# Kernel tuning notes

Hardware: AMD Instinct MI355X
Metric: run time of the kernel (lower is better)

Reference implementation:

```python
import jax, jax.numpy as jnp
import numpy as np

B, N, NF, K, C, L, IN_DIM, FC_DIM, OUT_DIM = 4, 4096, 8192, 512, 128, 4, 3, 128, 1


def setup_inputs() -> dict:
    rng = np.random.default_rng(0)
    key = jax.random.key(0)
    ks = jax.random.split(key, 10)
    # active-point indices inside the padded grid (unique, sorted) and matching mask
    ind = np.sort(rng.choice(NF, size=N, replace=False)).astype(np.int32)
    grid = rng.uniform(0.0, 2.0 * np.pi, size=(B, NF, 2)).astype(np.float32)
    w_quad = np.full((B, NF, 1), 1.0 / N, dtype=np.float32)
    mask = np.zeros((B, NF, 1), dtype=np.float32)
    mask[:, ind, 0] = 1.0
    xf = jnp.asarray(np.concatenate([grid, w_quad, mask], axis=-1))  # (B, NF, 4)
    x = jax.random.normal(ks[0], (B, N, IN_DIM), jnp.float32)
    modes = jnp.asarray(rng.integers(-16, 17, size=(K, 2)).astype(np.float32))
    scale = 1.0 / (C * C)
    wc = scale * jax.random.uniform(ks[1], (L, C, C, K), jnp.float32)
    ws_ = scale * jax.random.uniform(ks[2], (L, C, C, K), jnp.float32)
    w0 = scale * jax.random.uniform(ks[3], (L, C, C, 1), jnp.float32)
    conv_w = 0.05 * jax.random.normal(ks[4], (L, C, C), jnp.float32)
    conv_b = jnp.zeros((L, C), jnp.float32)
    fc0_w = 0.05 * jax.random.normal(ks[5], (IN_DIM, C), jnp.float32)
    fc0_b = jnp.zeros((C,), jnp.float32)
    fc1_w = 0.05 * jax.random.normal(ks[6], (C, FC_DIM), jnp.float32)
    fc1_b = jnp.zeros((FC_DIM,), jnp.float32)
    fc2_w = 0.05 * jax.random.normal(ks[7], (FC_DIM, OUT_DIM), jnp.float32)
    fc2_b = jnp.zeros((OUT_DIM,), jnp.float32)
    return dict(x=x, xf=xf, ind=jnp.asarray(ind), modes=modes,
                fc0_w=fc0_w, fc0_b=fc0_b, wc=wc, ws_=ws_, w0=w0,
                conv_w=conv_w, conv_b=conv_b, fc1_w=fc1_w, fc1_b=fc1_b,
                fc2_w=fc2_w, fc2_b=fc2_b)


def _gelu(v):
    # torch F.gelu default is the exact (erf) gelu
    return jax.nn.gelu(v, approximate=False)


def reference(x, xf, ind, modes, fc0_w, fc0_b, wc, ws_, w0, conv_w, conv_b,
              fc1_w, fc1_b, fc2_w, fc2_b):
    ndim = modes.shape[1]
    aux = jnp.transpose(xf[..., -2 - ndim:], (0, 2, 1))      # (B, ndim+2, NF)
    grid = aux[:, :ndim]                                       # (B, ndim, NF)
    wq = aux[:, ndim:ndim + 1]                                 # (B, 1, NF) quadrature weights
    temp = jnp.einsum('bdx,kd->bkx', grid, modes)              # (B, K, NF)
    bases_c, bases_s = jnp.cos(temp), jnp.sin(temp)
    bases_0 = jnp.ones((xf.shape[0], 1, xf.shape[1]), xf.dtype)
    size = ind.shape[0]                                        # count_nonzero(mask) == len(ind)
    wb_c = bases_c * (wq * size)
    wb_s = bases_s * (wq * size)
    wb_0 = bases_0 * (wq * size)
    # lift and scatter active points into the padded grid (done ONCE, as in the original)
    h = jnp.einsum('bni,ic->bcn', x[..., :fc0_w.shape[0]], fc0_w) + fc0_b[None, :, None]
    xg = jnp.zeros((x.shape[0], h.shape[1], xf.shape[1]), h.dtype).at[:, :, ind].set(h)
    nf = xg.shape[-1]
    n_layers = wc.shape[0]
    for i in range(n_layers):
        # forward non-uniform Fourier transform
        xch = jnp.einsum('bix,bkx->bik', xg, wb_c)
        xsh = -jnp.einsum('bix,bkx->bik', xg, wb_s)
        x0h = jnp.einsum('bix,bkx->bik', xg, wb_0)
        wci, wsi, w0i = wc[i] / nf, ws_[i] / nf, w0[i] / nf
        # complex-style mode mixing
        fch = jnp.einsum('bik,iok->bok', xch, wci) - jnp.einsum('bik,iok->bok', xsh, wsi)
        fsh = jnp.einsum('bik,iok->bok', xsh, wci) + jnp.einsum('bik,iok->bok', xch, wsi)
        f0h = jnp.einsum('bik,iok->bok', x0h, w0i)
        # inverse transform, then gather active points
        x1 = (jnp.einsum('bok,bkx->box', f0h, bases_0)
              + 2.0 * jnp.einsum('bok,bkx->box', fch, bases_c)
              - 2.0 * jnp.einsum('bok,bkx->box', fsh, bases_s))[:, :, ind]
        # 1x1 conv skip path on active points
        x2 = jnp.einsum('oi,bin->bon', conv_w[i], h) + conv_b[i][None, :, None]
        h = x1 + x2
        if i != n_layers - 1:
            h = _gelu(h)
    out = jnp.transpose(h, (0, 2, 1))                          # (B, N, C)
    out = _gelu(out @ fc1_w + fc1_b)
    out = out @ fc2_w + fc2_b                                  # (B, N, 1)
    return out
```

## Files before the change

### kernel.cpp

```cpp
#include <hip/hip_runtime.h>
#include <cmath>

#define B_ 4
#define N_ 4096
#define NF_ 8192
#define K_ 512
#define C_ 128
#define L_ 4
#define FCD_ 128
#define SPLIT_ 8

typedef _Float16 f16x8 __attribute__((ext_vector_type(8)));
typedef _Float16 f16x4 __attribute__((ext_vector_type(4)));
typedef float f32x4 __attribute__((ext_vector_type(4)));

#define MFMA16(a, b, c) __builtin_amdgcn_mfma_f32_16x16x32_f16((a), (b), (c), 0, 0, 0)

static const float SPLIT_SCALE = 2048.0f;
static const float INV_SPLIT_SCALE = 1.0f / 2048.0f;

static const size_t SZ_H   = (size_t)B_ * C_ * N_;
static const size_t SZ_HS  = (size_t)B_ * C_ * N_ / 2;
static const size_t SZ_FS  = (size_t)B_ * C_ * K_ / 2;
static const size_t SZ_CW  = (size_t)L_ * C_ * C_ / 2;
static const size_t SZ_W1  = (size_t)C_ * FCD_ / 2;

static const size_t H_OFF    = 0;
static const size_t H2_OFF   = H_OFF + SZ_H;
static const size_t HAH_OFF  = H2_OFF + SZ_H;
static const size_t HAL_OFF  = HAH_OFF + SZ_HS;
static const size_t HTH_OFF  = HAL_OFF + SZ_HS;
static const size_t HTL_OFF  = HTH_OFF + SZ_HS;
static const size_t WQN_OFF  = HTL_OFF + SZ_HS;
static const size_t GXY_OFF  = WQN_OFF + (size_t)B_ * N_;
static const size_t XCH_OFF  = GXY_OFF + (size_t)B_ * N_ * 2;
static const size_t XSH_OFF  = XCH_OFF + (size_t)B_ * C_ * K_;
static const size_t FCHH_OFF = XSH_OFF + (size_t)B_ * C_ * K_;
static const size_t FCHL_OFF = FCHH_OFF + SZ_FS;
static const size_t FSHH_OFF = FCHL_OFF + SZ_FS;
static const size_t FSHL_OFF = FSHH_OFF + SZ_FS;
static const size_t CWH_OFF  = FSHL_OFF + SZ_FS;
static const size_t CWL_OFF  = CWH_OFF + SZ_CW;
static const size_t X0_OFF   = CWL_OFF + SZ_CW;
static const size_t F0_OFF   = X0_OFF + (size_t)B_ * C_;
static const size_t XCP_OFF  = F0_OFF + (size_t)B_ * C_;
static const size_t XSP_OFF  = XCP_OFF + (size_t)SPLIT_ * B_ * C_ * K_;
static const size_t W1TH_OFF = XSP_OFF + (size_t)SPLIT_ * B_ * C_ * K_;
static const size_t W1TL_OFF = W1TH_OFF + SZ_W1;

__device__ __forceinline__ float gelu_exact(float v) {
    return v * 0.5f * (1.0f + erff(v * 0.70710678118654752440f));
}

__device__ __forceinline__ void fsplit(float v, _Float16& hi, _Float16& lo) {
    hi = (_Float16)v;
    lo = (_Float16)((v - (float)hi) * SPLIT_SCALE);
}

__global__ void prep_kernel(const float* __restrict__ x, const float* __restrict__ xf,
                            const int* __restrict__ ind, const float* __restrict__ fc0_w,
                            const float* __restrict__ fc0_b, float* __restrict__ h,
                            float* __restrict__ wqn, float* __restrict__ gxy) {
    int n = blockIdx.x * 256 + threadIdx.x;
    int c = blockIdx.y;
    int b = blockIdx.z;
    const float* xp = x + ((size_t)b * N_ + n) * 3;
    float acc = fc0_b[c] + xp[0] * fc0_w[0 * C_ + c] + xp[1] * fc0_w[1 * C_ + c]
              + xp[2] * fc0_w[2 * C_ + c];
    h[((size_t)b * C_ + c) * N_ + n] = acc;
    if (c == 0) {
        int g = ind[n];
        const float* xfp = xf + ((size_t)b * NF_ + g) * 4;
        wqn[b * N_ + n] = xfp[2] * (float)N_;
        gxy[((size_t)b * N_ + n) * 2 + 0] = xfp[0];
        gxy[((size_t)b * N_ + n) * 2 + 1] = xfp[1];
    }
}

__global__ void conv_split(const float* __restrict__ conv_w, _Float16* __restrict__ cwh,
                           _Float16* __restrict__ cwl) {
    int t = blockIdx.x * 256 + threadIdx.x;
    _Float16 hi, lo;
    fsplit(conv_w[t], hi, lo);
    cwh[t] = hi; cwl[t] = lo;
}

__global__ void w1_split(const float* __restrict__ fc1_w, _Float16* __restrict__ w1th,
                         _Float16* __restrict__ w1tl) {
    int t = blockIdx.x * 256 + threadIdx.x;
    int j = t >> 7, c = t & (C_ - 1);
    _Float16 hi, lo;
    fsplit(fc1_w[c * FCD_ + j], hi, lo);
    w1th[t] = hi; w1tl[t] = lo;
}

__device__ __forceinline__ unsigned int pack2(_Float16 a, _Float16 b) {
    union { _Float16 f[2]; unsigned int u; } x;
    x.f[0] = a; x.f[1] = b;
    return x.u;
}

__device__ __forceinline__ void unpack2(unsigned int v, _Float16& a, _Float16& b) {
    union { _Float16 f[2]; unsigned int u; } x;
    x.u = v;
    a = x.f[0]; b = x.f[1];
}

__global__ __launch_bounds__(256) void split_h(const float* __restrict__ h,
        const float* __restrict__ wqn, _Float16* __restrict__ hah,
        _Float16* __restrict__ hal, _Float16* __restrict__ hth,
        _Float16* __restrict__ htl) {
    __shared__ unsigned int pk[64][65];
    int tid = threadIdx.x;
    int n0 = blockIdx.x * 64, c0 = blockIdx.y * 64, b = blockIdx.z;
    int col = tid & 63, row4 = tid >> 6;
    for (int r = row4; r < 64; r += 4) {
        int c = c0 + r, n = n0 + col;
        float v = h[((size_t)b * C_ + c) * N_ + n];
        _Float16 ph, pl;
        fsplit(v, ph, pl);
        pk[r][col] = pack2(ph, pl);
        float a = v * wqn[b * N_ + n];
        _Float16 ah, al;
        fsplit(a, ah, al);
        size_t o = ((size_t)b * C_ + c) * N_ + n;
        hah[o] = ah; hal[o] = al;
    }
    __syncthreads();
    for (int r = row4; r < 64; r += 4) {
        int n = n0 + r, c = c0 + col;
        _Float16 ph, pl;
        unpack2(pk[col][r], ph, pl);
        size_t o = ((size_t)b * N_ + n) * C_ + c;
        hth[o] = ph; htl[o] = pl;
    }
}

__global__ __launch_bounds__(256) void fwd_mfma(const _Float16* __restrict__ hah,
        const _Float16* __restrict__ hal, const float* __restrict__ gxy,
        const float* __restrict__ modes, float* __restrict__ xcp,
        float* __restrict__ xsp) {
    __shared__ __align__(16) _Float16 tCH[2][32][40];
    __shared__ __align__(16) _Float16 tCL[2][32][40];
    __shared__ __align__(16) _Float16 tSH[2][32][40];
    __shared__ __align__(16) _Float16 tSL[2][32][40];
    __shared__ float gx_s[N_ / SPLIT_], gy_s[N_ / SPLIT_];
    int tid = threadIdx.x;
    int w = tid >> 6, lane = tid & 63, l15 = lane & 15, q = lane >> 4;
    int k0g = blockIdx.x * 32, p = blockIdx.y, b = blockIdx.z;
    int cstrip = w * 32;
    {
        const float* g = gxy + ((size_t)b * N_ + p * (N_ / SPLIT_)) * 2;
        float4 v = *(const float4*)(g + tid * 4);
        gx_s[tid * 2 + 0] = v.x; gy_s[tid * 2 + 0] = v.y;
        gx_s[tid * 2 + 1] = v.z; gy_s[tid * 2 + 1] = v.w;
    }
    int kk = tid & 31, ng = tid >> 5;
    float mx = modes[(k0g + kk) * 2 + 0];
    float my = modes[(k0g + kk) * 2 + 1];

    size_t arow[2];
    arow[0] = ((size_t)b * C_ + cstrip + l15) * N_;
    arow[1] = arow[0] + (size_t)16 * N_;
    f32x4 z = {0.f, 0.f, 0.f, 0.f};
    f32x4 aC1[2][2], aC2[2][2], aS1[2][2], aS2[2][2];
    for (int i = 0; i < 2; ++i)
        for (int j = 0; j < 2; ++j) {
            aC1[i][j] = z; aC2[i][j] = z; aS1[i][j] = z; aS2[i][j] = z;
        }

#define FWD_TILE(ITER, BUF) do {                                             \
        int nb_ = (ITER) * 32;                                               \
        f16x4 vch_, vcl_, vsh_, vsl_;                                        \
        for (int j_ = 0; j_ < 4; ++j_) {                                     \
            int nn_ = ng * 4 + j_;                                           \
            float t_ = gx_s[nb_ + nn_] * mx + gy_s[nb_ + nn_] * my;          \
            float s_, c_;                                                    \
            sincosf(t_, &s_, &c_);                                           \
            _Float16 h_, lo_;                                                \
            fsplit(c_, h_, lo_); vch_[j_] = h_; vcl_[j_] = lo_;              \
            fsplit(s_, h_, lo_); vsh_[j_] = h_; vsl_[j_] = lo_;              \
        }                                                                    \
        *(f16x4*)&tCH[BUF][kk][ng * 4] = vch_;                               \
        *(f16x4*)&tCL[BUF][kk][ng * 4] = vcl_;                               \
        *(f16x4*)&tSH[BUF][kk][ng * 4] = vsh_;                               \
        *(f16x4*)&tSL[BUF][kk][ng * 4] = vsl_;                               \
    } while (0)

    __syncthreads();
    FWD_TILE(0, 0);
    const int NIT = (N_ / SPLIT_) / 32;
    for (int it = 0; it < NIT; ++it) {
        __syncthreads();
        int cur = it & 1;
        int off = p * (N_ / SPLIT_) + it * 32 + q * 8;
        f16x8 ah[2], al[2];
        for (int mt = 0; mt < 2; ++mt) {
            ah[mt] = *(const f16x8*)(hah + arow[mt] + off);
            al[mt] = *(const f16x8*)(hal + arow[mt] + off);
        }
        f16x8 bch[2], bcl[2], bsh[2], bsl[2];
        for (int kt = 0; kt < 2; ++kt) {
            int r = kt * 16 + l15;
            bch[kt] = *(const f16x8*)&tCH[cur][r][q * 8];
            bcl[kt] = *(const f16x8*)&tCL[cur][r][q * 8];
            bsh[kt] = *(const f16x8*)&tSH[cur][r][q * 8];
            bsl[kt] = *(const f16x8*)&tSL[cur][r][q * 8];
        }
        if (it + 1 < NIT) FWD_TILE(it + 1, cur ^ 1);
        for (int mt = 0; mt < 2; ++mt)
            for (int kt = 0; kt < 2; ++kt) {
                aC1[mt][kt] = MFMA16(ah[mt], bch[kt], aC1[mt][kt]);
                aC2[mt][kt] = MFMA16(ah[mt], bcl[kt], aC2[mt][kt]);
                aC2[mt][kt] = MFMA16(al[mt], bch[kt], aC2[mt][kt]);
                aS1[mt][kt] = MFMA16(ah[mt], bsh[kt], aS1[mt][kt]);
                aS2[mt][kt] = MFMA16(ah[mt], bsl[kt], aS2[mt][kt]);
                aS2[mt][kt] = MFMA16(al[mt], bsh[kt], aS2[mt][kt]);
            }
    }
#undef FWD_TILE
    size_t pb = (size_t)p * B_ + b;
    for (int mt = 0; mt < 2; ++mt)
        for (int kt = 0; kt < 2; ++kt)
            for (int r = 0; r < 4; ++r) {
                int c = cstrip + mt * 16 + q * 4 + r;
                int k = k0g + kt * 16 + l15;
                size_t o = (pb * C_ + c) * K_ + k;
                xcp[o] = aC1[mt][kt][r] + aC2[mt][kt][r] * INV_SPLIT_SCALE;
                xsp[o] = -(aS1[mt][kt][r] + aS2[mt][kt][r] * INV_SPLIT_SCALE);
            }
}

__global__ void red_kernel(const float* __restrict__ xcp, const float* __restrict__ xsp,
                           float* __restrict__ xch, float* __restrict__ xsh) {
    int t = blockIdx.x * 256 + threadIdx.x;
    const int BCK = B_ * C_ * K_;
    float a = 0.f, s = 0.f;
    for (int p = 0; p < SPLIT_; ++p) {
        a += xcp[(size_t)p * BCK + t];
        s += xsp[(size_t)p * BCK + t];
    }
    xch[t] = a; xsh[t] = s;
}

__global__ void x0_kernel(const float* __restrict__ h, const float* __restrict__ wqn,
                          float* __restrict__ x0h) {
    int c = blockIdx.x, b = blockIdx.y;
    int tid = threadIdx.x;
    const float* hp = h + ((size_t)b * C_ + c) * N_;
    const float* wq = wqn + b * N_;
    float a = 0.f;
    for (int n = tid; n < N_; n += 256) a += hp[n] * wq[n];
    __shared__ float red[4];
    for (int off = 32; off; off >>= 1) a += __shfl_down(a, off, 64);
    if ((tid & 63) == 0) red[tid >> 6] = a;
    __syncthreads();
    if (tid == 0) x0h[b * C_ + c] = red[0] + red[1] + red[2] + red[3];
}

__global__ void f0_kernel(const float* __restrict__ x0h, const float* __restrict__ w0,
                          int l, float* __restrict__ f0h) {
    int o = threadIdx.x, b = blockIdx.x;
    const float* w = w0 + (size_t)l * C_ * C_;
    float a = 0.f;
    for (int i = 0; i < C_; ++i) a += x0h[b * C_ + i] * w[i * C_ + o];
    f0h[b * C_ + o] = a * (1.0f / NF_);
}

__global__ __launch_bounds__(256) void mix_kernel(const float* __restrict__ xch,
        const float* __restrict__ xsh, const float* __restrict__ wc,
        const float* __restrict__ ws, int l, _Float16* __restrict__ fchh,
        _Float16* __restrict__ fchl, _Float16* __restrict__ fshh,
        _Float16* __restrict__ fshl) {
    __shared__ float red[512 * 5];
    int tid = threadIdx.x;
    int lane = tid & 63;
    int g = tid >> 6;
    int k = blockIdx.x * 64 + lane;
    int o = blockIdx.y;
    const float* wcb = wc + ((size_t)l * C_ * C_ + o) * K_ + k;
    const float* wsb = ws + ((size_t)l * C_ * C_ + o) * K_ + k;
    float fc[4] = {0, 0, 0, 0}, fs[4] = {0, 0, 0, 0};
    int i0 = g * 32;
#pragma unroll 4
    for (int ii = 0; ii < 32; ++ii) {
        int i = i0 + ii;
        float wci = wcb[(size_t)i * (C_ * K_)];
        float wsi = wsb[(size_t)i * (C_ * K_)];
#pragma unroll
        for (int b = 0; b < 4; ++b) {
            float xc = xch[((size_t)b * C_ + i) * K_ + k];
            float xs = xsh[((size_t)b * C_ + i) * K_ + k];
            fc[b] += xc * wci - xs * wsi;
            fs[b] += xs * wci + xc * wsi;
        }
    }
#pragma unroll
    for (int b = 0; b < 4; ++b) {
        red[((b * 2 + 0) * 64 + lane) * 5 + g] = fc[b];
        red[((b * 2 + 1) * 64 + lane) * 5 + g] = fs[b];
    }
    __syncthreads();
    const float sc = 2.0f / NF_;
    for (int v = tid; v < 512; v += 256) {
        float sum = (red[v * 5 + 0] + red[v * 5 + 1] + red[v * 5 + 2] + red[v * 5 + 3]) * sc;
        int lane2 = v & 63;
        int bs = v >> 6;
        int b = bs >> 1, s = bs & 1;
        size_t idx = ((size_t)b * C_ + o) * K_ + blockIdx.x * 64 + lane2;
        _Float16 hi, lo;
        if (s == 0) {
            fsplit(sum, hi, lo);
            fchh[idx] = hi; fchl[idx] = lo;
        } else {
            fsplit(-sum, hi, lo);
            fshh[idx] = hi; fshl[idx] = lo;
        }
    }
}

__global__ __launch_bounds__(256) void inv_mfma(const _Float16* __restrict__ fchh,
        const _Float16* __restrict__ fchl, const _Float16* __restrict__ fshh,
        const _Float16* __restrict__ fshl, const float* __restrict__ gxy,
        const float* __restrict__ modes, const _Float16* __restrict__ cwh,
        const _Float16* __restrict__ cwl, const _Float16* __restrict__ hth,
        const _Float16* __restrict__ htl, const float* __restrict__ f0h,
        const float* __restrict__ conv_b, int l, int last, float* __restrict__ hnext) {
    __shared__ __align__(16) _Float16 tCH[2][32][40];
    __shared__ __align__(16) _Float16 tCL[2][32][40];
    __shared__ __align__(16) _Float16 tSH[2][32][40];
    __shared__ __align__(16) _Float16 tSL[2][32][40];
    __shared__ float mx_s[K_], my_s[K_];
    int tid = threadIdx.x;
    int w = tid >> 6, lane = tid & 63, l15 = lane & 15, q = lane >> 4;
    int n0g = blockIdx.x * 32, b = blockIdx.y;
    int cstrip = w * 32;
    {
        float4 v = *(const float4*)(modes + tid * 4);
        mx_s[tid * 2 + 0] = v.x; my_s[tid * 2 + 0] = v.y;
        mx_s[tid * 2 + 1] = v.z; my_s[tid * 2 + 1] = v.w;
    }
    int nn = tid & 31, kg = tid >> 5;
    float gx = gxy[((size_t)b * N_ + n0g + nn) * 2 + 0];
    float gy = gxy[((size_t)b * N_ + n0g + nn) * 2 + 1];

    size_t frow[2], nrow2[2], crow[2];
    frow[0] = ((size_t)b * C_ + cstrip + l15) * K_;
    frow[1] = frow[0] + (size_t)16 * K_;
    nrow2[0] = ((size_t)b * N_ + n0g + l15) * C_;
    nrow2[1] = nrow2[0] + (size_t)16 * C_;
    crow[0] = ((size_t)l * C_ + cstrip + l15) * C_;
    crow[1] = crow[0] + (size_t)16 * C_;
    f32x4 z = {0.f, 0.f, 0.f, 0.f};
    f32x4 a1[2][2], a2[2][2];
    for (int i = 0; i < 2; ++i)
        for (int j = 0; j < 2; ++j) { a1[i][j] = z; a2[i][j] = z; }

#define INV_TILE(KC, BUF) do {                                               \
        f16x4 vch_, vcl_, vsh_, vsl_;                                        \
        for (int j_ = 0; j_ < 4; ++j_) {                                     \
            int kk_ = (KC) + kg * 4 + j_;                                    \
            float t_ = gx * mx_s[kk_] + gy * my_s[kk_];                      \
            float s_, c_;                                                    \
            sincosf(t_, &s_, &c_);                                           \
            _Float16 h_, lo_;                                                \
            fsplit(c_, h_, lo_); vch_[j_] = h_; vcl_[j_] = lo_;              \
            fsplit(s_, h_, lo_); vsh_[j_] = h_; vsl_[j_] = lo_;              \
        }                                                                    \
        *(f16x4*)&tCH[BUF][nn][kg * 4] = vch_;                               \
        *(f16x4*)&tCL[BUF][nn][kg * 4] = vcl_;                               \
        *(f16x4*)&tSH[BUF][nn][kg * 4] = vsh_;                               \
        *(f16x4*)&tSL[BUF][nn][kg * 4] = vsl_;                               \
    } while (0)

    __syncthreads();
    INV_TILE(0, 0);
    const int NIT = K_ / 32;
    for (int it = 0; it < NIT; ++it) {
        __syncthreads();
        int cur = it & 1;
        int off = it * 32 + q * 8;
        f16x8 fch_[2], fcl_[2], fsh_[2], fsl_[2];
        for (int mt = 0; mt < 2; ++mt) {
            fch_[mt] = *(const f16x8*)(fchh + frow[mt] + off);
            fcl_[mt] = *(const f16x8*)(fchl + frow[mt] + off);
            fsh_[mt] = *(const f16x8*)(fshh + frow[mt] + off);
            fsl_[mt] = *(const f16x8*)(fshl + frow[mt] + off);
        }
        f16x8 bch[2], bcl[2], bsh[2], bsl[2];
        for (int nt = 0; nt < 2; ++nt) {
            int r = nt * 16 + l15;
            bch[nt] = *(const f16x8*)&tCH[cur][r][q * 8];
            bcl[nt] = *(const f16x8*)&tCL[cur][r][q * 8];
            bsh[nt] = *(const f16x8*)&tSH[cur][r][q * 8];
            bsl[nt] = *(const f16x8*)&tSL[cur][r][q * 8];
        }
        if (it + 1 < NIT) INV_TILE((it + 1) * 32, cur ^ 1);
        for (int mt = 0; mt < 2; ++mt)
            for (int nt = 0; nt < 2; ++nt) {
                a1[mt][nt] = MFMA16(fch_[mt], bch[nt], a1[mt][nt]);
                a2[mt][nt] = MFMA16(fch_[mt], bcl[nt], a2[mt][nt]);
                a2[mt][nt] = MFMA16(fcl_[mt], bch[nt], a2[mt][nt]);
                a1[mt][nt] = MFMA16(fsh_[mt], bsh[nt], a1[mt][nt]);
                a2[mt][nt] = MFMA16(fsh_[mt], bsl[nt], a2[mt][nt]);
                a2[mt][nt] = MFMA16(fsl_[mt], bsh[nt], a2[mt][nt]);
            }
    }
#undef INV_TILE
    for (int ic = 0; ic < C_; ic += 32) {
        int off = ic + q * 8;
        f16x8 awh[2], awl[2];
        for (int mt = 0; mt < 2; ++mt) {
            awh[mt] = *(const f16x8*)(cwh + crow[mt] + off);
            awl[mt] = *(const f16x8*)(cwl + crow[mt] + off);
        }
        f16x8 bhh[2], bhl[2];
        for (int nt = 0; nt < 2; ++nt) {
            bhh[nt] = *(const f16x8*)(hth + nrow2[nt] + off);
            bhl[nt] = *(const f16x8*)(htl + nrow2[nt] + off);
        }
        for (int mt = 0; mt < 2; ++mt)
            for (int nt = 0; nt < 2; ++nt) {
                a1[mt][nt] = MFMA16(awh[mt], bhh[nt], a1[mt][nt]);
                a2[mt][nt] = MFMA16(awh[mt], bhl[nt], a2[mt][nt]);
                a2[mt][nt] = MFMA16(awl[mt], bhh[nt], a2[mt][nt]);
            }
    }
    for (int mt = 0; mt < 2; ++mt)
        for (int nt = 0; nt < 2; ++nt)
            for (int r = 0; r < 4; ++r) {
                int c = cstrip + mt * 16 + q * 4 + r;
                int n = n0g + nt * 16 + l15;
                float v = a1[mt][nt][r] + a2[mt][nt][r] * INV_SPLIT_SCALE
                        + f0h[b * C_ + c] + conv_b[l * C_ + c];
                if (!last) v = gelu_exact(v);
                hnext[((size_t)b * C_ + c) * N_ + n] = v;
            }
}

__global__ __launch_bounds__(256) void head_mfma(const _Float16* __restrict__ hth,
        const _Float16* __restrict__ htl, const _Float16* __restrict__ w1th,
        const _Float16* __restrict__ w1tl, const float* __restrict__ fc1_b,
        const float* __restrict__ fc2_w, const float* __restrict__ fc2_b,
        float* __restrict__ out) {
    __shared__ float red[4][4][2][16];
    int tid = threadIdx.x;
    int w = tid >> 6, lane = tid & 63, l15 = lane & 15, q = lane >> 4;
    int n0 = blockIdx.x * 32, b = blockIdx.y;
    int jstrip = w * 32;
    size_t wrow[2], hrow[2];
    wrow[0] = (size_t)(jstrip + l15) * C_;
    wrow[1] = wrow[0] + (size_t)16 * C_;
    hrow[0] = ((size_t)b * N_ + n0 + l15) * C_;
    hrow[1] = hrow[0] + (size_t)16 * C_;
    f32x4 z = {0.f, 0.f, 0.f, 0.f};
    f32x4 a1[2][2], a2[2][2];
    for (int i = 0; i < 2; ++i)
        for (int j = 0; j < 2; ++j) { a1[i][j] = z; a2[i][j] = z; }
    for (int cc = 0; cc < C_; cc += 32) {
        int off = cc + q * 8;
        f16x8 ah[2], al[2], bh[2], bl[2];
        for (int mt = 0; mt < 2; ++mt) {
            ah[mt] = *(const f16x8*)(w1th + wrow[mt] + off);
            al[mt] = *(const f16x8*)(w1tl + wrow[mt] + off);
        }
        for (int nt = 0; nt < 2; ++nt) {
            bh[nt] = *(const f16x8*)(hth + hrow[nt] + off);
            bl[nt] = *(const f16x8*)(htl + hrow[nt] + off);
        }
        for (int mt = 0; mt < 2; ++mt)
            for (int nt = 0; nt < 2; ++nt) {
                a1[mt][nt] = MFMA16(ah[mt], bh[nt], a1[mt][nt]);
                a2[mt][nt] = MFMA16(ah[mt], bl[nt], a2[mt][nt]);
                a2[mt][nt] = MFMA16(al[mt], bh[nt], a2[mt][nt]);
            }
    }
    float p[2] = {0.f, 0.f};
    for (int mt = 0; mt < 2; ++mt)
        for (int nt = 0; nt < 2; ++nt)
            for (int r = 0; r < 4; ++r) {
                int j = jstrip + mt * 16 + q * 4 + r;
                float v = a1[mt][nt][r] + a2[mt][nt][r] * INV_SPLIT_SCALE + fc1_b[j];
                p[nt] += gelu_exact(v) * fc2_w[j];
            }
    red[w][q][0][l15] = p[0];
    red[w][q][1][l15] = p[1];
    __syncthreads();
    if (tid < 32) {
        int nt = tid >> 4, nl = tid & 15;
        float s = 0.f;
        for (int ww = 0; ww < 4; ++ww)
            for (int qq = 0; qq < 4; ++qq) s += red[ww][qq][nt][nl];
        out[(size_t)b * N_ + n0 + nt * 16 + nl] = s + fc2_b[0];
    }
}

extern "C" void kernel_launch(void* const* d_in, const int* in_sizes, int n_in,
                              void* d_out, int out_size, void* d_ws, size_t ws_size,
                              hipStream_t stream) {
    const float* x      = (const float*)d_in[0];
    const float* xf     = (const float*)d_in[1];
    const int*   ind    = (const int*)d_in[2];
    const float* modes  = (const float*)d_in[3];
    const float* fc0_w  = (const float*)d_in[4];
    const float* fc0_b  = (const float*)d_in[5];
    const float* wc     = (const float*)d_in[6];
    const float* ws     = (const float*)d_in[7];
    const float* w0     = (const float*)d_in[8];
    const float* conv_w = (const float*)d_in[9];
    const float* conv_b = (const float*)d_in[10];
    const float* fc1_w  = (const float*)d_in[11];
    const float* fc1_b  = (const float*)d_in[12];
    const float* fc2_w  = (const float*)d_in[13];
    const float* fc2_b  = (const float*)d_in[14];
    float* out = (float*)d_out;

    float* wsf = (float*)d_ws;
    float* h   = wsf + H_OFF;
    float* h2  = wsf + H2_OFF;
    _Float16* hah = (_Float16*)(wsf + HAH_OFF);
    _Float16* hal = (_Float16*)(wsf + HAL_OFF);
    _Float16* hth = (_Float16*)(wsf + HTH_OFF);
    _Float16* htl = (_Float16*)(wsf + HTL_OFF);
    float* wqn = wsf + WQN_OFF;
    float* gxy = wsf + GXY_OFF;
    float* xch = wsf + XCH_OFF;
    float* xsh = wsf + XSH_OFF;
    _Float16* fchh = (_Float16*)(wsf + FCHH_OFF);
    _Float16* fchl = (_Float16*)(wsf + FCHL_OFF);
    _Float16* fshh = (_Float16*)(wsf + FSHH_OFF);
    _Float16* fshl = (_Float16*)(wsf + FSHL_OFF);
    _Float16* cwh = (_Float16*)(wsf + CWH_OFF);
    _Float16* cwl = (_Float16*)(wsf + CWL_OFF);
    float* x0h = wsf + X0_OFF;
    float* f0h = wsf + F0_OFF;
    float* xcp = wsf + XCP_OFF;
    float* xsp = wsf + XSP_OFF;
    _Float16* w1th = (_Float16*)(wsf + W1TH_OFF);
    _Float16* w1tl = (_Float16*)(wsf + W1TL_OFF);

    prep_kernel<<<dim3(N_ / 256, C_, B_), 256, 0, stream>>>(x, xf, ind, fc0_w, fc0_b,
                                                            h, wqn, gxy);
    conv_split<<<dim3(L_ * C_ * C_ / 256), 256, 0, stream>>>(conv_w, cwh, cwl);
    w1_split<<<dim3(C_ * FCD_ / 256), 256, 0, stream>>>(fc1_w, w1th, w1tl);

    float* cur = h;
    float* nxt = h2;
    for (int l = 0; l < L_; ++l) {
        split_h<<<dim3(N_ / 64, C_ / 64, B_), 256, 0, stream>>>(cur, wqn, hah, hal, hth, htl);
        fwd_mfma<<<dim3(K_ / 32, SPLIT_, B_), 256, 0, stream>>>(hah, hal, gxy, modes,
                                                                xcp, xsp);
        red_kernel<<<dim3(B_ * C_ * K_ / 256), 256, 0, stream>>>(xcp, xsp, xch, xsh);
        x0_kernel<<<dim3(C_, B_), 256, 0, stream>>>(cur, wqn, x0h);
        f0_kernel<<<dim3(B_), C_, 0, stream>>>(x0h, w0, l, f0h);
        mix_kernel<<<dim3(K_ / 64, C_), 256, 0, stream>>>(xch, xsh, wc, ws, l,
                                                          fchh, fchl, fshh, fshl);
        inv_mfma<<<dim3(N_ / 32, B_), 256, 0, stream>>>(fchh, fchl, fshh, fshl,
            gxy, modes, cwh, cwl, hth, htl, f0h, conv_b, l,
            (l == L_ - 1) ? 1 : 0, nxt);
        float* t = cur; cur = nxt; nxt = t;
    }
    split_h<<<dim3(N_ / 64, C_ / 64, B_), 256, 0, stream>>>(cur, wqn, hah, hal, hth, htl);
    head_mfma<<<dim3(N_ / 32, B_), 256, 0, stream>>>(hth, htl, w1th, w1tl,
                                                     fc1_b, fc2_w, fc2_b, out);
}
```

Measured before the change: 765.9 us.

## Fuse split_h into inv_mfma epilogue and merge the weight-split kernels

The inverse-transform kernel now writes its output directly as the fp16 hi/lo split pieces. It produces both the transposed (n-major) copy and the quadrature-weighted copy the next layer needs. This removes the separate split_h pass after each layer and before the head, so the fp32 activations are no longer re-read. The conv and fc1 weight split kernels are also merged into a single launch. In exchange, the epilogue does stride-C fp16 scattered stores. It also overwrites hth/htl in place, which relies on each block reading and writing only its own rows and on the added barrier.

```diff
diff --git a/kernel.cpp b/kernel.cpp
--- a/kernel.cpp
+++ b/kernel.cpp
@@ -77,21 +77,22 @@
     }
 }
 
-__global__ void conv_split(const float* __restrict__ conv_w, _Float16* __restrict__ cwh,
-                           _Float16* __restrict__ cwl) {
+__global__ void weights_split(const float* __restrict__ conv_w,
+                              const float* __restrict__ fc1_w,
+                              _Float16* __restrict__ cwh, _Float16* __restrict__ cwl,
+                              _Float16* __restrict__ w1th, _Float16* __restrict__ w1tl) {
     int t = blockIdx.x * 256 + threadIdx.x;
+    const int NCW = L_ * C_ * C_;
     _Float16 hi, lo;
-    fsplit(conv_w[t], hi, lo);
-    cwh[t] = hi; cwl[t] = lo;
-}
-
-__global__ void w1_split(const float* __restrict__ fc1_w, _Float16* __restrict__ w1th,
-                         _Float16* __restrict__ w1tl) {
-    int t = blockIdx.x * 256 + threadIdx.x;
-    int j = t >> 7, c = t & (C_ - 1);
-    _Float16 hi, lo;
-    fsplit(fc1_w[c * FCD_ + j], hi, lo);
-    w1th[t] = hi; w1tl[t] = lo;
+    if (t < NCW) {
+        fsplit(conv_w[t], hi, lo);
+        cwh[t] = hi; cwl[t] = lo;
+    } else {
+        int u = t - NCW;
+        int j = u >> 7, c = u & (C_ - 1);
+        fsplit(fc1_w[c * FCD_ + j], hi, lo);
+        w1th[u] = hi; w1tl[u] = lo;
+    }
 }
 
 __device__ __forceinline__ unsigned int pack2(_Float16 a, _Float16 b) {
@@ -323,9 +324,12 @@
         const _Float16* __restrict__ fchl, const _Float16* __restrict__ fshh,
         const _Float16* __restrict__ fshl, const float* __restrict__ gxy,
         const float* __restrict__ modes, const _Float16* __restrict__ cwh,
-        const _Float16* __restrict__ cwl, const _Float16* __restrict__ hth,
-        const _Float16* __restrict__ htl, const float* __restrict__ f0h,
-        const float* __restrict__ conv_b, int l, int last, float* __restrict__ hnext) {
+        const _Float16* __restrict__ cwl, const _Float16* hth,
+        const _Float16* htl, const float* __restrict__ f0h,
+        const float* __restrict__ conv_b, const float* __restrict__ wqn,
+        int l, int last, float* __restrict__ hnext,
+        _Float16* __restrict__ oah, _Float16* __restrict__ oal,
+        _Float16* oth, _Float16* otl) {
     __shared__ __align__(16) _Float16 tCH[2][32][40];
     __shared__ __align__(16) _Float16 tCL[2][32][40];
     __shared__ __align__(16) _Float16 tSH[2][32][40];
@@ -426,6 +430,10 @@
                 a2[mt][nt] = MFMA16(awl[mt], bhh[nt], a2[mt][nt]);
             }
     }
+    __syncthreads();
+    float wq2[2];
+    wq2[0] = wqn[b * N_ + n0g + l15];
+    wq2[1] = wqn[b * N_ + n0g + 16 + l15];
     for (int mt = 0; mt < 2; ++mt)
         for (int nt = 0; nt < 2; ++nt)
             for (int r = 0; r < 4; ++r) {
@@ -434,7 +442,18 @@
                 float v = a1[mt][nt][r] + a2[mt][nt][r] * INV_SPLIT_SCALE
                         + f0h[b * C_ + c] + conv_b[l * C_ + c];
                 if (!last) v = gelu_exact(v);
-                hnext[((size_t)b * C_ + c) * N_ + n] = v;
+                size_t onc = ((size_t)b * N_ + n) * C_ + c;
+                _Float16 ph, pl;
+                fsplit(v, ph, pl);
+                oth[onc] = ph; otl[onc] = pl;
+                if (!last) {
+                    size_t ocn = ((size_t)b * C_ + c) * N_ + n;
+                    hnext[ocn] = v;
+                    float a = v * wq2[nt];
+                    _Float16 ah, al;
+                    fsplit(a, ah, al);
+                    oah[ocn] = ah; oal[ocn] = al;
+                }
             }
 }
 
@@ -541,13 +560,13 @@
 
     prep_kernel<<<dim3(N_ / 256, C_, B_), 256, 0, stream>>>(x, xf, ind, fc0_w, fc0_b,
                                                             h, wqn, gxy);
-    conv_split<<<dim3(L_ * C_ * C_ / 256), 256, 0, stream>>>(conv_w, cwh, cwl);
-    w1_split<<<dim3(C_ * FCD_ / 256), 256, 0, stream>>>(fc1_w, w1th, w1tl);
+    weights_split<<<dim3((L_ * C_ * C_ + C_ * FCD_) / 256), 256, 0, stream>>>(
+        conv_w, fc1_w, cwh, cwl, w1th, w1tl);
+    split_h<<<dim3(N_ / 64, C_ / 64, B_), 256, 0, stream>>>(h, wqn, hah, hal, hth, htl);
 
     float* cur = h;
     float* nxt = h2;
     for (int l = 0; l < L_; ++l) {
-        split_h<<<dim3(N_ / 64, C_ / 64, B_), 256, 0, stream>>>(cur, wqn, hah, hal, hth, htl);
         fwd_mfma<<<dim3(K_ / 32, SPLIT_, B_), 256, 0, stream>>>(hah, hal, gxy, modes,
                                                                 xcp, xsp);
         red_kernel<<<dim3(B_ * C_ * K_ / 256), 256, 0, stream>>>(xcp, xsp, xch, xsh);
@@ -556,11 +575,10 @@
         mix_kernel<<<dim3(K_ / 64, C_), 256, 0, stream>>>(xch, xsh, wc, ws, l,
                                                           fchh, fchl, fshh, fshl);
         inv_mfma<<<dim3(N_ / 32, B_), 256, 0, stream>>>(fchh, fchl, fshh, fshl,
-            gxy, modes, cwh, cwl, hth, htl, f0h, conv_b, l,
-            (l == L_ - 1) ? 1 : 0, nxt);
+            gxy, modes, cwh, cwl, hth, htl, f0h, conv_b, wqn, l,
+            (l == L_ - 1) ? 1 : 0, nxt, hah, hal, hth, htl);
         float* t = cur; cur = nxt; nxt = t;
     }
-    split_h<<<dim3(N_ / 64, C_ / 64, B_), 256, 0, stream>>>(cur, wqn, hah, hal, hth, htl);
     head_mfma<<<dim3(N_ / 32, B_), 256, 0, stream>>>(hth, htl, w1th, w1tl,
                                                      fc1_b, fc2_w, fc2_b, out);
 }
```

Result: faster. 750.3 us (-2.0%).
